# Optimization experiments

Hardware: AMD Instinct MI355X
Metric: run time of the kernel (lower is better)

Reference implementation:

```python
import jax, jax.numpy as jnp
import numpy as np

DROPOUT_P = 0.1
HEAD_DIM = 64
INV_SCALE = 1.0 / float(np.sqrt(HEAD_DIM))  # matches driver: inv_scale = 1/head_dim**0.5


def setup_inputs() -> dict:
    key = jax.random.key(0)
    k1, k2, k3, k4 = jax.random.split(key, 4)
    B, S, H, D = 2, 2048, 16, HEAD_DIM
    return {
        "query": jax.random.normal(k1, (B, S, H, D), dtype=jnp.float32),
        "key": jax.random.normal(k2, (B, S, H, D), dtype=jnp.float32),
        "value": jax.random.normal(k3, (B, S, H, D), dtype=jnp.float32),
        "attn_mask": jnp.zeros((B, H, S, S), dtype=jnp.float32),
        "dropout_u": jax.random.uniform(k4, (B, H, S, S), dtype=jnp.float32),
    }


def reference(query, key, value, attn_mask, dropout_u):
    # [B,S,H,D] -> [B,H,S,D]
    q = jnp.transpose(query, (0, 2, 1, 3))
    k = jnp.transpose(key, (0, 2, 1, 3))
    v = jnp.transpose(value, (0, 2, 1, 3))
    # scores = (q @ k^T) / inv_scale + mask   (faithful: original .div(inv_scale))
    scores = jnp.einsum("bhqd,bhkd->bhqk", q, k) / INV_SCALE + attn_mask
    attn = jax.nn.softmax(scores, axis=-1)
    # deterministic dropout: keep where u >= p, scale by 1/(1-p)
    keep = (dropout_u >= DROPOUT_P).astype(attn.dtype) / (1.0 - DROPOUT_P)
    out = jnp.einsum("bhqk,bhkd->bhqd", attn * keep, v)  # [B,H,S,D]
    return out
```

## Files before the change

kernel.cpp:

```cpp
#include <hip/hip_runtime.h>
#include <stdint.h>

#define S_LEN 2048
#define HEADS 16
#define DIM   64

typedef float  f4v  __attribute__((ext_vector_type(4)));
typedef float  f2v  __attribute__((ext_vector_type(2)));
typedef float  f16v __attribute__((ext_vector_type(16)));
typedef short  s8v  __attribute__((ext_vector_type(8)));
typedef unsigned int   u4v  __attribute__((ext_vector_type(4)));
typedef unsigned short us4v __attribute__((ext_vector_type(4)));

#define LOGC 0.105360516f

__device__ __forceinline__ unsigned short f2bf(float f) {
  unsigned int u = __float_as_uint(f);
  u += 0x7fffu + ((u >> 16) & 1u);
  return (unsigned short)(u >> 16);
}
__device__ __forceinline__ float bf2f(unsigned short h) {
  return __uint_as_float(((unsigned int)h) << 16);
}
__device__ __forceinline__ unsigned int pk2(float e0, float e1) {
  return (unsigned int)f2bf(e0) | ((unsigned int)f2bf(e1) << 16);
}

__global__ __launch_bounds__(256) void prep_k(const float* __restrict__ K,
                                              unsigned short* __restrict__ Khf,
                                              unsigned short* __restrict__ Klf) {
  int f = blockIdx.x * 256 + threadIdx.x;
  int l  = f & 63;
  int dc = (f >> 6) & 3;
  int kt = (f >> 8) & 63;
  int bh = f >> 14;
  int b = bh >> 4, hh = bh & 15;
  int s  = kt * 32 + (l & 31);
  int d0 = dc * 16 + (l >> 5) * 8;
  const float* src = K + (((size_t)(b * S_LEN + s) * HEADS + hh) << 6) + d0;
  f4v va = *(const f4v*)src;
  f4v vb = *(const f4v*)(src + 4);
  us4v ha, hb, la, lb;
#pragma unroll
  for (int i = 0; i < 4; ++i) {
    unsigned short h = f2bf(va[i]);
    ha[i] = h; la[i] = f2bf(va[i] - bf2f(h));
    unsigned short h2 = f2bf(vb[i]);
    hb[i] = h2; lb[i] = f2bf(vb[i] - bf2f(h2));
  }
  size_t o = (size_t)f * 8;
  *(us4v*)(Khf + o) = ha; *(us4v*)(Khf + o + 4) = hb;
  *(us4v*)(Klf + o) = la; *(us4v*)(Klf + o + 4) = lb;
}

__global__ __launch_bounds__(256) void prep_v(const float* __restrict__ V,
                                              unsigned short* __restrict__ Vf) {
  __shared__ float tile[32 * 68];
  int bh = blockIdx.x >> 6;
  int kt = blockIdx.x & 63;
  int b = bh >> 4, hh = bh & 15;
  int t = threadIdx.x;
  {
    int row = t >> 3, c8 = (t & 7) * 8;
    const float* src =
        V + (((size_t)(b * S_LEN + kt * 32 + row) * HEADS + hh) << 6) + c8;
    f4v va = *(const f4v*)src;
    f4v vb = *(const f4v*)(src + 4);
    *(f4v*)(tile + row * 68 + c8) = va;
    *(f4v*)(tile + row * 68 + c8 + 4) = vb;
  }
  __syncthreads();
  int kc = t >> 7, dblk = (t >> 6) & 1, l = t & 63;
  int s0 = kc * 16 + (l >> 5) * 8;
  int col = dblk * 32 + (l & 31);
  us4v w0, w1;
#pragma unroll
  for (int j = 0; j < 4; ++j) {
    w0[j] = f2bf(tile[(s0 + j) * 68 + col]);
    w1[j] = f2bf(tile[(s0 + 4 + j) * 68 + col]);
  }
  size_t o = ((((size_t)bh * 64 + kt) * 4 + kc * 2 + dblk) * 64 + l) * 8;
  *(us4v*)(Vf + o) = w0;
  *(us4v*)(Vf + o + 4) = w1;
}

template <int PARTIAL>
__global__ __launch_bounds__(256, 2) void attn_fwd(
    const float* __restrict__ Q, const float* __restrict__ MASK,
    const float* __restrict__ U, const unsigned short* __restrict__ Khf,
    const unsigned short* __restrict__ Klf, const unsigned short* __restrict__ Vf,
    float* __restrict__ OUT, float* __restrict__ OPART, float* __restrict__ ML) {
  __shared__ float S_lds[4][1024];
  int bid = blockIdx.x;
  int bh, qt, sp;
  if (PARTIAL) {
    int lid = ((bid & 7) << 7) + (bid >> 3);
    bh = lid >> 5; qt = (lid >> 1) & 15; sp = lid & 1;
  } else {
    int lid = ((bid & 7) << 6) + (bid >> 3);
    bh = lid >> 4; qt = lid & 15; sp = 0;
  }
  const int NT = PARTIAL ? (S_LEN / 64) : (S_LEN / 32);
  const int kv_begin = PARTIAL ? sp * (S_LEN / 2) : 0;

  int wv = threadIdx.x >> 6, ln = threadIdx.x & 63;
  int l31 = ln & 31, h5 = ln >> 5;
  int q0 = qt * 128 + wv * 32;
  int b = bh >> 4, hh = bh & 15;
  float* lds = &S_lds[wv][0];

  const float* qrow = Q + (((size_t)(b * S_LEN + q0 + l31) * HEADS + hh) << 6);
  s8v qfh[4], qfl[4];
#pragma unroll
  for (int dc = 0; dc < 4; ++dc) {
    const float* p = qrow + dc * 16 + 8 * h5;
    f4v va = *(const f4v*)p;
    f4v vb = *(const f4v*)(p + 4);
    u4v wh, wl;
#pragma unroll
    for (int t = 0; t < 4; ++t) {
      float x0 = (t < 2) ? va[2 * t] : vb[2 * (t - 2)];
      float x1 = (t < 2) ? va[2 * t + 1] : vb[2 * (t - 2) + 1];
      unsigned short h0 = f2bf(x0), h1 = f2bf(x1);
      wh[t] = (unsigned)h0 | ((unsigned)h1 << 16);
      wl[t] = pk2(x0 - bf2f(h0), x1 - bf2f(h1));
    }
    qfh[dc] = __builtin_bit_cast(s8v, wh);
    qfl[dc] = __builtin_bit_cast(s8v, wl);
  }

  const float* Mp = MASK + ((size_t)bh << 22);
  const float* Up = U + ((size_t)bh << 22);
  const int vbase = (q0 + 4 * h5) * S_LEN + kv_begin + l31;

  const unsigned short* kbh = Khf + ((size_t)bh << 17) + ((size_t)kv_begin << 6);
  const unsigned short* kbl = Klf + ((size_t)bh << 17) + ((size_t)kv_begin << 6);
  const unsigned short* vbp = Vf + ((size_t)bh << 17) + ((size_t)kv_begin << 6);
  const int fl8 = ln * 8;

  f16v o0, o1;
#pragma unroll
  for (int i = 0; i < 16; ++i) { o0[i] = 0.f; o1[i] = 0.f; }
  float mrs = -3.0e38f;
  float pl  = 0.f;

  for (int kt = 0; kt < NT; ++kt) {
    int kv0 = kt << 5;
    s8v kfh[4], kfl[4];
#pragma unroll
    for (int dc = 0; dc < 4; ++dc) {
      size_t off = (size_t)((kt * 4 + dc) << 9) + fl8;
      kfh[dc] = *(const s8v*)(kbh + off);
      kfl[dc] = *(const s8v*)(kbl + off);
    }
    s8v vf[2][2];
#pragma unroll
    for (int kc = 0; kc < 2; ++kc)
#pragma unroll
      for (int db = 0; db < 2; ++db)
        vf[kc][db] = *(const s8v*)(vbp + (size_t)((kt * 4 + kc * 2 + db) << 9) + fl8);
    float mk[16], uk[16];
#pragma unroll
    for (int r = 0; r < 16; ++r) {
      int off = vbase + kv0 + (8 * (r >> 2) + (r & 3)) * S_LEN;
      mk[r] = Mp[off];
      uk[r] = Up[off];
    }
    f16v sc;
#pragma unroll
    for (int i = 0; i < 16; ++i) sc[i] = 0.f;
#pragma unroll
    for (int dc = 0; dc < 4; ++dc) {
      sc = __builtin_amdgcn_mfma_f32_32x32x16_bf16(qfh[dc], kfh[dc], sc, 0, 0, 0);
      sc = __builtin_amdgcn_mfma_f32_32x32x16_bf16(qfl[dc], kfh[dc], sc, 0, 0, 0);
      sc = __builtin_amdgcn_mfma_f32_32x32x16_bf16(qfh[dc], kfl[dc], sc, 0, 0, 0);
    }
#pragma unroll
    for (int r = 0; r < 16; ++r) {
      float sv = fmaf(sc[r], 8.0f, mk[r]);
      unsigned bits = (__float_as_uint(sv) & ~1u) | (uk[r] < 0.1f ? 1u : 0u);
      int qr = 8 * (r >> 2) + 4 * h5 + (r & 3);
      lds[qr * 32 + (((((l31 >> 2) ^ (qr & 7)) << 2)) | (l31 & 3))] =
          __uint_as_float(bits);
    }
    __builtin_amdgcn_sched_barrier(0);
    f4v sq[4];
#pragma unroll
    for (int cc = 0; cc < 4; ++cc) {
      int c = (cc >> 1) * 4 + (cc & 1) + 2 * h5;
      sq[cc] = *(const f4v*)(lds + l31 * 32 + ((c ^ (l31 & 7)) << 2));
    }
    float tm = -3.0e38f;
#pragma unroll
    for (int cc = 0; cc < 4; ++cc)
#pragma unroll
      for (int w = 0; w < 4; ++w) tm = fmaxf(tm, sq[cc][w]);
    float tmax = fmaxf(tm, __shfl_xor(tm, 32));
    if (__any(tmax > mrs + (8.0f + LOGC))) {
      float mold = mrs + LOGC;
      float mn = fmaxf(mold, tmax);
      float al = __expf(mold - mn);
      mrs = mn - LOGC;
      pl *= al;
#pragma unroll
      for (int r = 0; r < 16; ++r) {
        float arow = __shfl(al, 8 * (r >> 2) + 4 * h5 + (r & 3));
        o0[r] *= arow; o1[r] *= arow;
      }
    }
    u4v pa0, pa1;
#pragma unroll
    for (int cc = 0; cc < 4; ++cc) {
      float p0 = __expf(sq[cc][0] - mrs), p1 = __expf(sq[cc][1] - mrs);
      float p2 = __expf(sq[cc][2] - mrs), p3 = __expf(sq[cc][3] - mrs);
      pl += (p0 + p1) + (p2 + p3);
      float d0 = (__float_as_uint(sq[cc][0]) & 1u) ? 0.f : p0;
      float d1 = (__float_as_uint(sq[cc][1]) & 1u) ? 0.f : p1;
      float d2 = (__float_as_uint(sq[cc][2]) & 1u) ? 0.f : p2;
      float d3 = (__float_as_uint(sq[cc][3]) & 1u) ? 0.f : p3;
      unsigned w0 = pk2(d0, d1), w1 = pk2(d2, d3);
      if (cc < 2) { pa0[2 * cc] = w0; pa0[2 * cc + 1] = w1; }
      else        { pa1[2 * (cc - 2)] = w0; pa1[2 * (cc - 2) + 1] = w1; }
    }
    s8v paA = __builtin_bit_cast(s8v, pa0), paB = __builtin_bit_cast(s8v, pa1);
    o0 = __builtin_amdgcn_mfma_f32_32x32x16_bf16(paA, vf[0][0], o0, 0, 0, 0);
    o0 = __builtin_amdgcn_mfma_f32_32x32x16_bf16(paB, vf[1][0], o0, 0, 0, 0);
    o1 = __builtin_amdgcn_mfma_f32_32x32x16_bf16(paA, vf[0][1], o1, 0, 0, 0);
    o1 = __builtin_amdgcn_mfma_f32_32x32x16_bf16(paB, vf[1][1], o1, 0, 0, 0);
  }

  pl += __shfl_xor(pl, 32);

  if (PARTIAL) {
    size_t rowbase = (size_t)bh * S_LEN + q0;
#pragma unroll
    for (int r = 0; r < 16; ++r) {
      int qr = 8 * (r >> 2) + 4 * h5 + (r & 3);
      float* p = OPART + (rowbase + qr) * 128 + sp * 64 + l31;
      p[0]  = o0[r];
      p[32] = o1[r];
    }
    if (h5 == 0) {
      f2v s; s[0] = mrs; s[1] = pl;
      *(f2v*)(ML + (rowbase + l31) * 4 + sp * 2) = s;
    }
  } else {
    float inv = 1.0f / (0.9f * pl);
#pragma unroll
    for (int r = 0; r < 16; ++r) {
      int qr = 8 * (r >> 2) + 4 * h5 + (r & 3);
      float invv = __shfl(inv, qr);
      float* orow = OUT + (((size_t)bh * S_LEN + q0 + qr) << 6) + l31;
      orow[0]  = o0[r] * invv;
      orow[32] = o1[r] * invv;
    }
  }
}

__global__ __launch_bounds__(256) void combine(const float* __restrict__ OPART,
                                               const float* __restrict__ ML,
                                               float* __restrict__ OUT) {
  int gid = blockIdx.x * 256 + threadIdx.x;
  size_t row = (size_t)(gid >> 4);
  int d4 = (gid & 15) * 4;
  f4v mlv = *(const f4v*)(ML + row * 4);
  float m0 = mlv[0], l0 = mlv[1], m1 = mlv[2], l1 = mlv[3];
  float M = fmaxf(m0, m1);
  float w0 = __expf(m0 - M), w1 = __expf(m1 - M);
  float inv = 1.0f / (0.9f * (l0 * w0 + l1 * w1));
  f4v a = *(const f4v*)(OPART + row * 128 + d4);
  f4v bb = *(const f4v*)(OPART + row * 128 + 64 + d4);
  f4v o;
#pragma unroll
  for (int i = 0; i < 4; ++i) o[i] = (a[i] * w0 + bb[i] * w1) * inv;
  *(f4v*)(OUT + row * 64 + d4) = o;
}

extern "C" void kernel_launch(void* const* d_in, const int* in_sizes, int n_in,
                              void* d_out, int out_size, void* d_ws, size_t ws_size,
                              hipStream_t stream) {
  const float* Q = (const float*)d_in[0];
  const float* K = (const float*)d_in[1];
  const float* V = (const float*)d_in[2];
  const float* M = (const float*)d_in[3];
  const float* U = (const float*)d_in[4];
  float* out = (float*)d_out;

  unsigned short* Khf = (unsigned short*)d_ws;
  unsigned short* Klf = Khf + (size_t)(4u << 20);
  unsigned short* Vf  = Klf + (size_t)(4u << 20);
  float* Opart = (float*)(Vf + (size_t)(4u << 20));
  float* ML    = Opart + (size_t)65536 * 128;
  const size_t need = (size_t)24 * 1024 * 1024 + (size_t)65536 * 132 * 4 + (1u << 20);

  prep_k<<<2048, 256, 0, stream>>>(K, Khf, Klf);
  prep_v<<<2048, 256, 0, stream>>>(V, Vf);
  if (ws_size >= need) {
    attn_fwd<1><<<1024, 256, 0, stream>>>(Q, M, U, Khf, Klf, Vf, out, Opart, ML);
    combine<<<4096, 256, 0, stream>>>(Opart, ML, out);
  } else {
    attn_fwd<0><<<512, 256, 0, stream>>>(Q, M, U, Khf, Klf, Vf, out, Opart, ML);
  }
}
```

Baseline: 276.7 us.

## Double-buffer mask and dropout tiles via direct global-to-LDS async loads

Replaces the per-lane scalar global loads of the mask and dropout-uniform values with global_load_lds transfers into a per-wave double-buffered LDS region, issued one KV tile ahead. The current tile's values are then read from LDS after the QK MFMAs, and the score scratch reuses the same buffer. The goal is to hide the memory latency of the bandwidth-heavy mask and dropout streams behind compute and to coalesce those reads. In exchange LDS use grows from 16KB to 64KB per block, which may limit occupancy. There is also no explicit vmcnt wait before the LDS reads, which relies on compiler or hardware ordering.

```diff
diff --git a/kernel.cpp b/kernel.cpp
--- a/kernel.cpp
+++ b/kernel.cpp
@@ -24,6 +24,12 @@
 }
 __device__ __forceinline__ unsigned int pk2(float e0, float e1) {
   return (unsigned int)f2bf(e0) | ((unsigned int)f2bf(e1) << 16);
+}
+
+__device__ __forceinline__ void glds16(const float* g, float* l) {
+  __builtin_amdgcn_global_load_lds(
+      (const __attribute__((address_space(1))) unsigned int*)g,
+      (__attribute__((address_space(3))) unsigned int*)l, 16, 0, 0);
 }
 
 __global__ __launch_bounds__(256) void prep_k(const float* __restrict__ K,
@@ -84,13 +90,24 @@
   *(us4v*)(Vf + o + 4) = w1;
 }
 
+#define PREFETCH_MU(KT, CB)                                                    \
+  {                                                                            \
+    int kvp = (KT) << 5;                                                       \
+    size_t rowb = (size_t)(q0 + (ln >> 3)) * S_LEN + kv_begin + kvp + 4 * (ln & 7); \
+    _Pragma("unroll") for (int i = 0; i < 4; ++i) {                            \
+      glds16(Mp + rowb + (size_t)(i * 8) * S_LEN, muw + (CB) * 2048 + i * 256);\
+      glds16(Up + rowb + (size_t)(i * 8) * S_LEN,                              \
+             muw + (CB) * 2048 + 1024 + i * 256);                              \
+    }                                                                          \
+  }
+
 template <int PARTIAL>
 __global__ __launch_bounds__(256, 2) void attn_fwd(
     const float* __restrict__ Q, const float* __restrict__ MASK,
     const float* __restrict__ U, const unsigned short* __restrict__ Khf,
     const unsigned short* __restrict__ Klf, const unsigned short* __restrict__ Vf,
     float* __restrict__ OUT, float* __restrict__ OPART, float* __restrict__ ML) {
-  __shared__ float S_lds[4][1024];
+  __shared__ __align__(16) float MU[4][2][2048];
   int bid = blockIdx.x;
   int bh, qt, sp;
   if (PARTIAL) {
@@ -107,7 +124,7 @@
   int l31 = ln & 31, h5 = ln >> 5;
   int q0 = qt * 128 + wv * 32;
   int b = bh >> 4, hh = bh & 15;
-  float* lds = &S_lds[wv][0];
+  float* muw = &MU[wv][0][0];
 
   const float* qrow = Q + (((size_t)(b * S_LEN + q0 + l31) * HEADS + hh) << 6);
   s8v qfh[4], qfl[4];
@@ -131,8 +148,6 @@
 
   const float* Mp = MASK + ((size_t)bh << 22);
   const float* Up = U + ((size_t)bh << 22);
-  const int vbase = (q0 + 4 * h5) * S_LEN + kv_begin + l31;
-
   const unsigned short* kbh = Khf + ((size_t)bh << 17) + ((size_t)kv_begin << 6);
   const unsigned short* kbl = Klf + ((size_t)bh << 17) + ((size_t)kv_begin << 6);
   const unsigned short* vbp = Vf + ((size_t)bh << 17) + ((size_t)kv_begin << 6);
@@ -144,8 +159,11 @@
   float mrs = -3.0e38f;
   float pl  = 0.f;
 
+  PREFETCH_MU(0, 0)
+
   for (int kt = 0; kt < NT; ++kt) {
-    int kv0 = kt << 5;
+    const int cb = kt & 1;
+    float* sbuf = muw + cb * 2048;
     s8v kfh[4], kfl[4];
 #pragma unroll
     for (int dc = 0; dc < 4; ++dc) {
@@ -159,13 +177,9 @@
 #pragma unroll
       for (int db = 0; db < 2; ++db)
         vf[kc][db] = *(const s8v*)(vbp + (size_t)((kt * 4 + kc * 2 + db) << 9) + fl8);
-    float mk[16], uk[16];
-#pragma unroll
-    for (int r = 0; r < 16; ++r) {
-      int off = vbase + kv0 + (8 * (r >> 2) + (r & 3)) * S_LEN;
-      mk[r] = Mp[off];
-      uk[r] = Up[off];
-    }
+    __builtin_amdgcn_sched_barrier(0);
+    if (kt + 1 < NT) PREFETCH_MU(kt + 1, cb ^ 1)
+    __builtin_amdgcn_sched_barrier(0);
     f16v sc;
 #pragma unroll
     for (int i = 0; i < 16; ++i) sc[i] = 0.f;
@@ -175,12 +189,21 @@
       sc = __builtin_amdgcn_mfma_f32_32x32x16_bf16(qfl[dc], kfh[dc], sc, 0, 0, 0);
       sc = __builtin_amdgcn_mfma_f32_32x32x16_bf16(qfh[dc], kfl[dc], sc, 0, 0, 0);
     }
+    __builtin_amdgcn_sched_barrier(0);
+    float mk[16], uk[16];
+#pragma unroll
+    for (int r = 0; r < 16; ++r) {
+      int qr = 8 * (r >> 2) + 4 * h5 + (r & 3);
+      mk[r] = sbuf[qr * 32 + l31];
+      uk[r] = sbuf[1024 + qr * 32 + l31];
+    }
+    __builtin_amdgcn_sched_barrier(0);
 #pragma unroll
     for (int r = 0; r < 16; ++r) {
       float sv = fmaf(sc[r], 8.0f, mk[r]);
       unsigned bits = (__float_as_uint(sv) & ~1u) | (uk[r] < 0.1f ? 1u : 0u);
       int qr = 8 * (r >> 2) + 4 * h5 + (r & 3);
-      lds[qr * 32 + (((((l31 >> 2) ^ (qr & 7)) << 2)) | (l31 & 3))] =
+      sbuf[qr * 32 + (((((l31 >> 2) ^ (qr & 7)) << 2)) | (l31 & 3))] =
           __uint_as_float(bits);
     }
     __builtin_amdgcn_sched_barrier(0);
@@ -188,7 +211,7 @@
 #pragma unroll
     for (int cc = 0; cc < 4; ++cc) {
       int c = (cc >> 1) * 4 + (cc & 1) + 2 * h5;
-      sq[cc] = *(const f4v*)(lds + l31 * 32 + ((c ^ (l31 & 7)) << 2));
+      sq[cc] = *(const f4v*)(sbuf + l31 * 32 + ((c ^ (l31 & 7)) << 2));
     }
     float tm = -3.0e38f;
 #pragma unroll
```

Result: no change. 274.2 us (-0.9%).

## Pre-pack dropout mask into bitmask words in a separate kernel

Applied to the files above, without the earlier changes.

Adds a prep_u kernel that reads the dropout uniform tensor with coalesced loads, tiles it through shared memory, and packs the keep/drop decision for 32 query rows into one 32-bit word per key column. The attention kernel then loads one uint per lane per KV tile instead of 16 strided float loads of U, easing scattered global loads in the main loop. In exchange it adds an extra full pass over U, a 16MB bitmask write and re-read, and more workspace.

```diff
diff --git a/kernel.cpp b/kernel.cpp
--- a/kernel.cpp
+++ b/kernel.cpp
@@ -84,10 +84,33 @@
   *(us4v*)(Vf + o + 4) = w1;
 }
 
+__global__ __launch_bounds__(256) void prep_u(const float* __restrict__ U,
+                                              unsigned int* __restrict__ UB) {
+  __shared__ float tile[32 * 260];
+  int cb = blockIdx.x & 7;
+  int qb = (blockIdx.x >> 3) & 63;
+  int bh = blockIdx.x >> 9;
+  const float* src =
+      U + ((size_t)bh << 22) + (size_t)(qb * 32) * S_LEN + cb * 256;
+  int t = threadIdx.x;
+  int row = t >> 3, c0 = (t & 7) * 32;
+#pragma unroll
+  for (int i = 0; i < 8; ++i) {
+    f4v v = *(const f4v*)(src + (size_t)row * S_LEN + c0 + i * 4);
+    *(f4v*)(tile + row * 260 + c0 + i * 4) = v;
+  }
+  __syncthreads();
+  unsigned w = 0;
+#pragma unroll
+  for (int r = 0; r < 32; ++r)
+    w |= (tile[r * 260 + t] >= 0.1f ? 1u : 0u) << r;
+  UB[((size_t)bh * 64 + qb) * 2048 + cb * 256 + t] = w;
+}
+
 template <int PARTIAL>
 __global__ __launch_bounds__(256, 2) void attn_fwd(
     const float* __restrict__ Q, const float* __restrict__ MASK,
-    const float* __restrict__ U, const unsigned short* __restrict__ Khf,
+    const unsigned int* __restrict__ UB, const unsigned short* __restrict__ Khf,
     const unsigned short* __restrict__ Klf, const unsigned short* __restrict__ Vf,
     float* __restrict__ OUT, float* __restrict__ OPART, float* __restrict__ ML) {
   __shared__ float S_lds[4][1024];
@@ -130,8 +153,9 @@
   }
 
   const float* Mp = MASK + ((size_t)bh << 22);
-  const float* Up = U + ((size_t)bh << 22);
   const int vbase = (q0 + 4 * h5) * S_LEN + kv_begin + l31;
+  const unsigned int* ubp =
+      UB + ((size_t)bh * 64 + (q0 >> 5)) * 2048 + kv_begin;
 
   const unsigned short* kbh = Khf + ((size_t)bh << 17) + ((size_t)kv_begin << 6);
   const unsigned short* kbl = Klf + ((size_t)bh << 17) + ((size_t)kv_begin << 6);
@@ -159,13 +183,11 @@
 #pragma unroll
       for (int db = 0; db < 2; ++db)
         vf[kc][db] = *(const s8v*)(vbp + (size_t)((kt * 4 + kc * 2 + db) << 9) + fl8);
-    float mk[16], uk[16];
-#pragma unroll
-    for (int r = 0; r < 16; ++r) {
-      int off = vbase + kv0 + (8 * (r >> 2) + (r & 3)) * S_LEN;
-      mk[r] = Mp[off];
-      uk[r] = Up[off];
-    }
+    unsigned int ub = ubp[kv0 + l31];
+    float mk[16];
+#pragma unroll
+    for (int r = 0; r < 16; ++r)
+      mk[r] = Mp[vbase + kv0 + (8 * (r >> 2) + (r & 3)) * S_LEN];
     f16v sc;
 #pragma unroll
     for (int i = 0; i < 16; ++i) sc[i] = 0.f;
@@ -178,8 +200,8 @@
 #pragma unroll
     for (int r = 0; r < 16; ++r) {
       float sv = fmaf(sc[r], 8.0f, mk[r]);
-      unsigned bits = (__float_as_uint(sv) & ~1u) | (uk[r] < 0.1f ? 1u : 0u);
       int qr = 8 * (r >> 2) + 4 * h5 + (r & 3);
+      unsigned bits = (__float_as_uint(sv) & ~1u) | (((ub >> qr) & 1u) ^ 1u);
       lds[qr * 32 + (((((l31 >> 2) ^ (qr & 7)) << 2)) | (l31 & 3))] =
           __uint_as_float(bits);
     }
@@ -289,16 +311,19 @@
   unsigned short* Khf = (unsigned short*)d_ws;
   unsigned short* Klf = Khf + (size_t)(4u << 20);
   unsigned short* Vf  = Klf + (size_t)(4u << 20);
-  float* Opart = (float*)(Vf + (size_t)(4u << 20));
+  unsigned int*   UB  = (unsigned int*)(Vf + (size_t)(4u << 20));
+  float* Opart = (float*)(UB + (size_t)(4u << 20));
   float* ML    = Opart + (size_t)65536 * 128;
-  const size_t need = (size_t)24 * 1024 * 1024 + (size_t)65536 * 132 * 4 + (1u << 20);
+  const size_t need =
+      (size_t)(24 + 16) * 1024 * 1024 + (size_t)65536 * 132 * 4 + (1u << 20);
 
   prep_k<<<2048, 256, 0, stream>>>(K, Khf, Klf);
   prep_v<<<2048, 256, 0, stream>>>(V, Vf);
+  prep_u<<<16384, 256, 0, stream>>>(U, UB);
   if (ws_size >= need) {
-    attn_fwd<1><<<1024, 256, 0, stream>>>(Q, M, U, Khf, Klf, Vf, out, Opart, ML);
+    attn_fwd<1><<<1024, 256, 0, stream>>>(Q, M, UB, Khf, Klf, Vf, out, Opart, ML);
     combine<<<4096, 256, 0, stream>>>(Opart, ML, out);
   } else {
-    attn_fwd<0><<<512, 256, 0, stream>>>(Q, M, U, Khf, Klf, Vf, out, Opart, ML);
-  }
-}
+    attn_fwd<0><<<512, 256, 0, stream>>>(Q, M, UB, Khf, Klf, Vf, out, Opart, ML);
+  }
+}
```

Result: slower. 301.5 us (+9.0%).
